# Kernel tuning notes

Measured on AMD Instinct MI355X. Metric: run time of the kernel, lower is better.

Reference implementation:

```python
import jax, jax.numpy as jnp
import numpy as np

N_NODES = 100000
N_EDGES = 3200000
IN_FEATS = 512
HIDDEN = 256
N_CLASSES = 64
NITER = 10
HALT_BIAS_INIT = 3.0


def setup_inputs() -> dict:
    key = jax.random.key(0)
    ks = jax.random.split(key, 8)
    x = jax.random.normal(ks[0], (N_NODES, IN_FEATS), dtype=jnp.float32)
    edge_index = jax.random.randint(ks[1], (2, N_EDGES), 0, N_NODES, dtype=jnp.int64)
    # Linear layers: layers[0]: in->hidden, layers[1]: hidden->classes, halt: classes->1
    W0 = jax.random.normal(ks[2], (IN_FEATS, HIDDEN), dtype=jnp.float32) / np.sqrt(IN_FEATS)
    b0 = jnp.zeros((HIDDEN,), dtype=jnp.float32)
    W1 = jax.random.normal(ks[3], (HIDDEN, N_CLASSES), dtype=jnp.float32) / np.sqrt(HIDDEN)
    b1 = jnp.zeros((N_CLASSES,), dtype=jnp.float32)
    Wh = jax.random.normal(ks[4], (N_CLASSES, 1), dtype=jnp.float32) / np.sqrt(N_CLASSES)
    bh = jnp.full((1,), HALT_BIAS_INIT, dtype=jnp.float32)
    return {"x": x, "edge_index": edge_index, "edge_dropout": 0,
            "W0": W0, "b0": b0, "W1": W1, "b1": b1, "Wh": Wh, "bh": bh}


def reference(x, edge_index, edge_dropout, W0, b0, W1, b1, Wh, bh):
    N = x.shape[0]
    # MLP encoder (eval mode: dropout is identity)
    h = jax.nn.relu(x @ W0 + b0)
    h = h @ W1 + b1                                   # [N, C]

    # gcn_norm with self-loops (edge_dropout=0 in eval => identical every iter)
    loops = jnp.arange(N, dtype=edge_index.dtype)
    row = jnp.concatenate([edge_index[0], loops])     # source
    col = jnp.concatenate([edge_index[1], loops])     # target (aggregation index)
    deg = jax.ops.segment_sum(jnp.ones_like(col, dtype=h.dtype), col, num_segments=N)
    dinv = jnp.where(deg > 0, deg ** -0.5, 0.0)
    norm = dinv[row] * dinv[col]                      # [E+N]

    def step(ph, _):
        msg = norm[:, None] * ph[row]                 # gather + scale, [E+N, C]
        ph2 = jax.ops.segment_sum(msg, col, num_segments=N)  # scatter_add
        logit = jnp.clip(ph2 @ Wh + bh, -10.0, 10.0)  # [N, 1]
        return ph2, (ph2, logit)

    _, (props, logits) = jax.lax.scan(step, h, None, length=NITER)
    outputs = jnp.concatenate([h[None], props], axis=0)       # [niter+1, N, C]
    halting_logits = jnp.transpose(logits[:, :, 0])           # [N, niter]

    lam = jax.nn.sigmoid(halting_logits)
    remain = jnp.cumprod(1.0 - lam, axis=1)                   # inclusive
    remain_excl = jnp.concatenate([jnp.ones((N, 1), lam.dtype), remain[:, :-1]], axis=1)
    p = lam * remain_excl
    p = p.at[:, -1].add(remain[:, -1])                        # leftover mass to last step
    return outputs, p, halting_logits
```

## Files before the change

### kernel.cpp

```cpp
#include <hip/hip_runtime.h>
#include <hip/hip_bf16.h>

#define N_NODES  100000
#define N_EDGES  3200000
#define IN_FEATS 512
#define HIDDEN   256
#define N_CLASSES 64
#define NITER    10

#define SCAN_NB  49

#define OUT_P_OFF  ((size_t)(NITER + 1) * N_NODES * N_CLASSES)
#define OUT_HL_OFF (OUT_P_OFF + (size_t)N_NODES * NITER)

#define WS_META_INTS (4 * N_NODES + 128)
#define WS_CSR_OFF   ((size_t)WS_META_INTS * 4)
#define WS_W0F_OFF   (WS_CSR_OFF + (size_t)2 * N_EDGES * 4)
#define WS_W1F_OFF   (WS_W0F_OFF + 262144)
#define WS_SH0_OFF   (WS_W1F_OFF + 32768)
#define WS_SH1_OFF   (WS_SH0_OFF + (size_t)N_NODES * 64 * 2)
#define WS_NEED_W    (WS_SH0_OFF)
#define WS_NEED_BF   (WS_SH1_OFF + (size_t)N_NODES * 64 * 2)

typedef _Float16 f16x8 __attribute__((ext_vector_type(8)));
typedef _Float16 f16x4 __attribute__((ext_vector_type(4)));
typedef float    f32x4 __attribute__((ext_vector_type(4)));

__device__ __forceinline__ float bflo(unsigned v) { return __uint_as_float(v << 16); }
__device__ __forceinline__ float bfhi(unsigned v) { return __uint_as_float(v & 0xffff0000u); }
__device__ __forceinline__ unsigned short f2bf(float f) {
    unsigned u = __float_as_uint(f);
    return (unsigned short)((u + 0x7fffu + ((u >> 16) & 1u)) >> 16);
}

__global__ void k_detect(const int* ei, int* flag) {
    if (threadIdx.x == 0 && blockIdx.x == 0) {
        int is64 = 1;
        for (int k = 0; k < 128; ++k) {
            if (ei[2 * k + 1] != 0) { is64 = 0; break; }
        }
        *flag = is64;
    }
}

__device__ __forceinline__ int edge_row(const void* ei, int is64, int e) {
    return is64 ? (int)((const long long*)ei)[e] : ((const int*)ei)[e];
}
__device__ __forceinline__ int edge_col(const void* ei, int is64, int e) {
    return is64 ? (int)((const long long*)ei)[(size_t)N_EDGES + e]
                : ((const int*)ei)[(size_t)N_EDGES + e];
}

__global__ void k_count(const void* ei, const int* flag, int* cnt) {
    int e = blockIdx.x * 256 + threadIdx.x;
    if (e >= N_EDGES) return;
    int is64 = *flag;
    atomicAdd(&cnt[edge_col(ei, is64, e)], 1);
}

__global__ __launch_bounds__(256) void k_scan1(const int* cnt, int* part) {
    __shared__ int sd[256];
    int b = blockIdx.x, t = threadIdx.x;
    int s = 0;
    for (int j = t; j < 2048; j += 256) {
        int idx = b * 2048 + j;
        if (idx < N_NODES) s += cnt[idx];
    }
    sd[t] = s;
    __syncthreads();
    for (int o = 128; o > 0; o >>= 1) {
        if (t < o) sd[t] += sd[t + o];
        __syncthreads();
    }
    if (t == 0) part[b] = sd[0];
}

__global__ __launch_bounds__(256) void k_scan2(int* part, int* offs) {
    __shared__ int sd[256];
    int t = threadIdx.x;
    sd[t] = (t < SCAN_NB) ? part[t] : 0;
    __syncthreads();
    for (int o = 1; o < 256; o <<= 1) {
        int add = (t >= o) ? sd[t - o] : 0;
        __syncthreads();
        sd[t] += add;
        __syncthreads();
    }
    if (t < SCAN_NB) part[t] = (t == 0) ? 0 : sd[t - 1];
    if (t == 0) offs[N_NODES] = N_EDGES;
}

__global__ __launch_bounds__(256) void k_scan3(const int* cnt, const int* part, int* offs) {
    __shared__ int sd[256];
    int b = blockIdx.x, t = threadIdx.x;
    int base = b * 2048 + t * 8;
    int local[8];
    int s = 0;
#pragma unroll
    for (int j = 0; j < 8; ++j) {
        int idx = base + j;
        int v = (idx < N_NODES) ? cnt[idx] : 0;
        local[j] = s;
        s += v;
    }
    sd[t] = s;
    __syncthreads();
    for (int o = 1; o < 256; o <<= 1) {
        int add = (t >= o) ? sd[t - o] : 0;
        __syncthreads();
        sd[t] += add;
        __syncthreads();
    }
    int tbase = part[b] + ((t == 0) ? 0 : sd[t - 1]);
#pragma unroll
    for (int j = 0; j < 8; ++j) {
        int idx = base + j;
        if (idx < N_NODES) offs[idx] = tbase + local[j];
    }
}

__global__ void k_dinv(const int* cnt, float* dinv) {
    int i = blockIdx.x * 256 + threadIdx.x;
    if (i >= N_NODES) return;
    dinv[i] = rsqrtf((float)(cnt[i] + 1));
}

__global__ void k_fill(const void* ei, const int* flag, const float* dinv,
                       const int* offs, int* cursor, int2* csr) {
    int e = blockIdx.x * 256 + threadIdx.x;
    if (e >= N_EDGES) return;
    int is64 = *flag;
    int r = edge_row(ei, is64, e);
    int c = edge_col(ei, is64, e);
    int pos = offs[c] + atomicAdd(&cursor[c], 1);
    csr[pos] = make_int2(r, __float_as_int(dinv[r] * dinv[c]));
}

__global__ void k_prep_w(const float* __restrict__ W0, const float* __restrict__ W1,
                         _Float16* __restrict__ W0f, _Float16* __restrict__ W1f) {
    int id = blockIdx.x * 256 + threadIdx.x;
    if (id < 16384) {
        int l = id & 63, c = (id >> 6) & 15, kkg = id >> 10;
        int n = c * 16 + (l & 15);
        int kb = kkg * 32 + ((l >> 4) * 8);
        f16x8 v;
#pragma unroll
        for (int j = 0; j < 8; ++j) v[j] = (_Float16)W0[(size_t)(kb + j) * HIDDEN + n];
        *(f16x8*)&W0f[(size_t)id * 8] = v;
    } else if (id < 16384 + 2048) {
        int id2 = id - 16384;
        int l = id2 & 63, c = (id2 >> 6) & 3, kkg = id2 >> 8;
        int n = c * 16 + (l & 15);
        int kb = kkg * 32 + ((l >> 4) * 8);
        f16x8 v;
#pragma unroll
        for (int j = 0; j < 8; ++j) v[j] = (_Float16)W1[(size_t)(kb + j) * N_CLASSES + n];
        *(f16x8*)&W1f[(size_t)id2 * 8] = v;
    }
}

#define EBM 64
#define XS_STRIDE 72
#define H1_STRIDE 264
#define XS0   0
#define XS1   9216
#define WST0  18432
#define WST1  34816
#define W2ST0 34816
#define W2ST1 38912
__global__ __launch_bounds__(256) void k_encoder_mfma(
        const float* __restrict__ x, const _Float16* __restrict__ W0f,
        const float* __restrict__ b0, const _Float16* __restrict__ W1f,
        const float* __restrict__ b1, float* __restrict__ out,
        unsigned short* __restrict__ shadow, int write_shadow) {
    __shared__ char smem[51200];
    const int t = threadIdx.x;
    const int w = t >> 6, l = t & 63;
    const int g = l >> 4, r15 = l & 15;
    const int row0 = blockIdx.x * EBM;
    const int c4 = t & 15;
    const int srow0 = t >> 4;

    f32x4 acc[16];
#pragma unroll
    for (int c = 0; c < 16; ++c) acc[c] = (f32x4){0.f, 0.f, 0.f, 0.f};

    float4 xld[4];
    f16x8 wld[4];
#pragma unroll
    for (int q = 0; q < 4; ++q) {
        int grow = row0 + q * 16 + srow0;
        if (grow >= N_NODES) grow = N_NODES - 1;
        xld[q] = *(const float4*)&x[(size_t)grow * IN_FEATS + c4 * 4];
    }
#pragma unroll
    for (int q = 0; q < 4; ++q) wld[q] = *(const f16x8*)&W0f[(size_t)(q * 256 + t) * 8];
#pragma unroll
    for (int q = 0; q < 4; ++q) {
        f16x4 hv = {(_Float16)xld[q].x, (_Float16)xld[q].y, (_Float16)xld[q].z, (_Float16)xld[q].w};
        *(f16x4*)(smem + XS0 + ((q * 16 + srow0) * XS_STRIDE + c4 * 4) * 2) = hv;
    }
#pragma unroll
    for (int q = 0; q < 4; ++q)
        *(f16x8*)(smem + WST0 + (q * 256 + t) * 16) = wld[q];
    __syncthreads();

    for (int kkg = 0; kkg < 16; ++kkg) {
        const int kc = kkg >> 1, kk = kkg & 1;
        if (kkg < 15) {
#pragma unroll
            for (int q = 0; q < 4; ++q)
                wld[q] = *(const f16x8*)&W0f[(size_t)((kkg + 1) * 1024 + q * 256 + t) * 8];
        }
        if (kk == 0 && kc < 7) {
#pragma unroll
            for (int q = 0; q < 4; ++q) {
                int grow = row0 + q * 16 + srow0;
                if (grow >= N_NODES) grow = N_NODES - 1;
                xld[q] = *(const float4*)&x[(size_t)grow * IN_FEATS + (kc + 1) * 64 + c4 * 4];
            }
        }
        const char* xbase = smem + ((kc & 1) ? XS1 : XS0);
        const char* wbase = smem + ((kkg & 1) ? WST1 : WST0);
        f16x8 af = *(const f16x8*)(xbase + ((w * 16 + r15) * XS_STRIDE + kk * 32 + g * 8) * 2);
#pragma unroll
        for (int c = 0; c < 16; ++c) {
            f16x8 bf = *(const f16x8*)(wbase + ((c << 6) | l) * 16);
            acc[c] = __builtin_amdgcn_mfma_f32_16x16x32_f16(af, bf, acc[c], 0, 0, 0);
        }
        if (kkg < 15) {
            char* wdst = smem + ((kkg & 1) ? WST0 : WST1);
#pragma unroll
            for (int q = 0; q < 4; ++q)
                *(f16x8*)(wdst + (q * 256 + t) * 16) = wld[q];
        }
        if (kk == 1 && kc < 7) {
            char* xdst = smem + ((kc & 1) ? XS0 : XS1);
#pragma unroll
            for (int q = 0; q < 4; ++q) {
                f16x4 hv = {(_Float16)xld[q].x, (_Float16)xld[q].y, (_Float16)xld[q].z, (_Float16)xld[q].w};
                *(f16x4*)(xdst + ((q * 16 + srow0) * XS_STRIDE + c4 * 4) * 2) = hv;
            }
        }
        __syncthreads();
    }

    f16x8 w2ld = *(const f16x8*)&W1f[(size_t)t * 8];
#pragma unroll
    for (int c = 0; c < 16; ++c) {
        float bb = b0[c * 16 + r15];
#pragma unroll
        for (int i = 0; i < 4; ++i) {
            int row = w * 16 + g * 4 + i;
            *(_Float16*)(smem + (row * H1_STRIDE + c * 16 + r15) * 2) =
                (_Float16)fmaxf(acc[c][i] + bb, 0.f);
        }
    }
    *(f16x8*)(smem + W2ST0 + t * 16) = w2ld;
    __syncthreads();

    f32x4 acc2[4];
#pragma unroll
    for (int c = 0; c < 4; ++c) acc2[c] = (f32x4){0.f, 0.f, 0.f, 0.f};
    for (int kkg = 0; kkg < 8; ++kkg) {
        if (kkg < 7) w2ld = *(const f16x8*)&W1f[(size_t)((kkg + 1) * 256 + t) * 8];
        const char* wbase = smem + ((kkg & 1) ? W2ST1 : W2ST0);
        f16x8 af = *(const f16x8*)(smem + ((w * 16 + r15) * H1_STRIDE + kkg * 32 + g * 8) * 2);
#pragma unroll
        for (int c = 0; c < 4; ++c) {
            f16x8 bf = *(const f16x8*)(wbase + ((c << 6) | l) * 16);
            acc2[c] = __builtin_amdgcn_mfma_f32_16x16x32_f16(af, bf, acc2[c], 0, 0, 0);
        }
        if (kkg < 7)
            *(f16x8*)(smem + ((kkg & 1) ? W2ST0 : W2ST1) + t * 16) = w2ld;
        __syncthreads();
    }
#pragma unroll
    for (int c = 0; c < 4; ++c) {
        float bb = b1[c * 16 + r15];
#pragma unroll
        for (int i = 0; i < 4; ++i) {
            int row = row0 + w * 16 + g * 4 + i;
            if (row < N_NODES) {
                float v = acc2[c][i] + bb;
                int col = c * 16 + r15;
                out[(size_t)row * 64 + col] = v;
                if (write_shadow) shadow[(size_t)row * 64 + col] = f2bf(v);
            }
        }
    }
}

__global__ __launch_bounds__(256) void k_encoder(const float* __restrict__ x,
        const float* __restrict__ W0, const float* __restrict__ b0,
        const float* __restrict__ W1, const float* __restrict__ b1,
        float* __restrict__ out) {
    __shared__ float xsh[32][128];
    __shared__ float h1s[32][HIDDEN + 1];
    const int t = threadIdx.x;
    const int rg = t >> 6;
    const int cg = t & 63;
    const size_t row0 = (size_t)blockIdx.x * 32;
    float acc[8][4];
#pragma unroll
    for (int i = 0; i < 8; ++i)
        acc[i][0] = acc[i][1] = acc[i][2] = acc[i][3] = 0.f;
    for (int kc = 0; kc < 4; ++kc) {
        __syncthreads();
#pragma unroll
        for (int q = 0; q < 4; ++q) {
            int idx = t + q * 256;
            int r = idx >> 5, pos = idx & 31;
            *(float4*)&xsh[r][pos * 4] =
                *(const float4*)&x[(row0 + r) * IN_FEATS + kc * 128 + pos * 4];
        }
        __syncthreads();
        for (int kk = 0; kk < 128; kk += 4) {
            float4 xv[8];
#pragma unroll
            for (int i = 0; i < 8; ++i) xv[i] = *(const float4*)&xsh[rg * 8 + i][kk];
#pragma unroll
            for (int j = 0; j < 4; ++j) {
                float4 wv = *(const float4*)&W0[(size_t)(kc * 128 + kk + j) * HIDDEN + cg * 4];
#pragma unroll
                for (int i = 0; i < 8; ++i) {
                    float xj = (&xv[i].x)[j];
                    acc[i][0] = fmaf(xj, wv.x, acc[i][0]);
                    acc[i][1] = fmaf(xj, wv.y, acc[i][1]);
                    acc[i][2] = fmaf(xj, wv.z, acc[i][2]);
                    acc[i][3] = fmaf(xj, wv.w, acc[i][3]);
                }
            }
        }
    }
    float4 bb = *(const float4*)&b0[cg * 4];
#pragma unroll
    for (int i = 0; i < 8; ++i) {
        int r = rg * 8 + i;
        h1s[r][cg * 4 + 0] = fmaxf(acc[i][0] + bb.x, 0.f);
        h1s[r][cg * 4 + 1] = fmaxf(acc[i][1] + bb.y, 0.f);
        h1s[r][cg * 4 + 2] = fmaxf(acc[i][2] + bb.z, 0.f);
        h1s[r][cg * 4 + 3] = fmaxf(acc[i][3] + bb.w, 0.f);
    }
    __syncthreads();
    float a2[8];
#pragma unroll
    for (int i = 0; i < 8; ++i) a2[i] = 0.f;
    for (int k = 0; k < HIDDEN; ++k) {
        float wv = W1[(size_t)k * N_CLASSES + cg];
#pragma unroll
        for (int i = 0; i < 8; ++i) a2[i] = fmaf(h1s[rg * 8 + i][k], wv, a2[i]);
    }
    float bv = b1[cg];
#pragma unroll
    for (int i = 0; i < 8; ++i)
        out[(row0 + rg * 8 + i) * N_CLASSES + cg] = a2[i] + bv;
}

__global__ __launch_bounds__(256) void k_prop_bf(
        const unsigned short* __restrict__ pin_bf, float* __restrict__ pout,
        unsigned short* __restrict__ pout_bf, const int* __restrict__ offs,
        const int2* __restrict__ csr, const float* __restrict__ dinv,
        const float* __restrict__ Wh, const float* __restrict__ bh,
        float* __restrict__ hl, int t) {
    int node = (blockIdx.x * 256 + threadIdx.x) >> 5;
    if (node >= N_NODES) return;
    int hlane = threadIdx.x & 31;
    int base = threadIdx.x & 32;
    float di = dinv[node];
    unsigned vs = *(const unsigned*)&pin_bf[(size_t)node * 64 + hlane * 2];
    float a0 = di * di * bflo(vs), a1 = di * di * bfhi(vs);
    float c0 = 0.f, c1 = 0.f;
    int e0 = offs[node], e1 = offs[node + 1];
    for (int eb = e0; eb < e1; eb += 32) {
        int n = e1 - eb; if (n > 32) n = 32;
        int idx = eb + hlane;
        int2 ew = csr[idx < e1 ? idx : e1 - 1];
        int j = 0;
        for (; j + 8 <= n; j += 8) {
            unsigned v[8]; float w[8];
#pragma unroll
            for (int q = 0; q < 8; ++q) {
                int s = __shfl(ew.x, base + j + q, 64);
                w[q] = __int_as_float(__shfl(ew.y, base + j + q, 64));
                v[q] = *(const unsigned*)&pin_bf[(size_t)s * 64 + hlane * 2];
            }
#pragma unroll
            for (int q = 0; q < 8; ++q) {
                if (q & 1) { c0 = fmaf(w[q], bflo(v[q]), c0); c1 = fmaf(w[q], bfhi(v[q]), c1); }
                else       { a0 = fmaf(w[q], bflo(v[q]), a0); a1 = fmaf(w[q], bfhi(v[q]), a1); }
            }
        }
        for (; j < n; ++j) {
            int s = __shfl(ew.x, base + j, 64);
            float w = __int_as_float(__shfl(ew.y, base + j, 64));
            unsigned v = *(const unsigned*)&pin_bf[(size_t)s * 64 + hlane * 2];
            a0 = fmaf(w, bflo(v), a0);
            a1 = fmaf(w, bfhi(v), a1);
        }
    }
    float fa = a0 + c0, fb = a1 + c1;
    *(float2*)&pout[(size_t)node * 64 + hlane * 2] = make_float2(fa, fb);
    *(unsigned*)&pout_bf[(size_t)node * 64 + hlane * 2] =
        (unsigned)f2bf(fa) | ((unsigned)f2bf(fb) << 16);
    float2 wh = *(const float2*)&Wh[hlane * 2];
    float s = fa * wh.x + fb * wh.y;
#pragma unroll
    for (int o = 16; o > 0; o >>= 1) s += __shfl_xor(s, o, 64);
    if (hlane == 0) {
        float lg = s + bh[0];
        lg = fminf(10.0f, fmaxf(-10.0f, lg));
        hl[(size_t)node * NITER + t] = lg;
    }
}

__global__ __launch_bounds__(256) void k_prop(const float* __restrict__ pin,
        float* __restrict__ pout, const int* __restrict__ offs,
        const int2* __restrict__ csr, const float* __restrict__ dinv,
        const float* __restrict__ Wh, const float* __restrict__ bh,
        float* __restrict__ hl, int t) {
    int wid = (blockIdx.x * blockDim.x + threadIdx.x) >> 6;
    int lane = threadIdx.x & 63;
    if (wid >= N_NODES) return;
    float di = dinv[wid];
    float a[4];
    a[0] = di * di * pin[(size_t)wid * 64 + lane];
    a[1] = a[2] = a[3] = 0.f;
    int e0 = offs[wid], e1 = offs[wid + 1];
    for (int eb = e0; eb < e1; eb += 64) {
        int n = e1 - eb; if (n > 64) n = 64;
        int idx = eb + lane;
        int2 ew = csr[idx < e1 ? idx : e1 - 1];
        int j = 0;
        for (; j + 8 <= n; j += 8) {
            float v[8], w[8];
#pragma unroll
            for (int q = 0; q < 8; ++q) {
                int s = __shfl(ew.x, j + q, 64);
                w[q] = __int_as_float(__shfl(ew.y, j + q, 64));
                v[q] = pin[(size_t)s * 64 + lane];
            }
#pragma unroll
            for (int q = 0; q < 8; ++q) a[q & 3] = fmaf(w[q], v[q], a[q & 3]);
        }
        for (; j < n; ++j) {
            int s = __shfl(ew.x, j, 64);
            float w = __int_as_float(__shfl(ew.y, j, 64));
            a[0] = fmaf(w, pin[(size_t)s * 64 + lane], a[0]);
        }
    }
    float acc = (a[0] + a[1]) + (a[2] + a[3]);
    pout[(size_t)wid * 64 + lane] = acc;
    float s = acc * Wh[lane];
#pragma unroll
    for (int o = 32; o > 0; o >>= 1) s += __shfl_xor(s, o, 64);
    if (lane == 0) {
        float lg = s + bh[0];
        lg = fminf(10.0f, fmaxf(-10.0f, lg));
        hl[(size_t)wid * NITER + t] = lg;
    }
}

__global__ void k_p(const float* __restrict__ hl, float* __restrict__ p) {
    int i = blockIdx.x * 256 + threadIdx.x;
    if (i >= N_NODES) return;
    float remain = 1.0f;
    float pv[NITER];
#pragma unroll
    for (int t = 0; t < NITER; ++t) {
        float lg = hl[(size_t)i * NITER + t];
        float lam = 1.0f / (1.0f + expf(-lg));
        pv[t] = lam * remain;
        remain *= (1.0f - lam);
    }
    pv[NITER - 1] += remain;
#pragma unroll
    for (int t = 0; t < NITER; ++t) p[(size_t)i * NITER + t] = pv[t];
}

extern "C" void kernel_launch(void* const* d_in, const int* in_sizes, int n_in,
                              void* d_out, int out_size, void* d_ws, size_t ws_size,
                              hipStream_t stream) {
    const float* x  = (const float*)d_in[0];
    const void*  ei = d_in[1];
    const float* W0 = (const float*)d_in[3];
    const float* b0 = (const float*)d_in[4];
    const float* W1 = (const float*)d_in[5];
    const float* b1 = (const float*)d_in[6];
    const float* Wh = (const float*)d_in[7];
    const float* bh = (const float*)d_in[8];
    float* out = (float*)d_out;

    int* ws_i   = (int*)d_ws;
    int* cnt    = ws_i;
    int* offs   = ws_i + N_NODES;
    int* cursor = ws_i + 2 * N_NODES + 2;
    int* part   = ws_i + 3 * N_NODES + 2;
    int* flag   = ws_i + 3 * N_NODES + 66;
    float* dinv = (float*)(ws_i + 3 * N_NODES + 128);
    int2* csr   = (int2*)((char*)d_ws + WS_CSR_OFF);
    _Float16* W0f = (_Float16*)((char*)d_ws + WS_W0F_OFF);
    _Float16* W1f = (_Float16*)((char*)d_ws + WS_W1F_OFF);
    unsigned short* sh0 = (unsigned short*)((char*)d_ws + WS_SH0_OFF);
    unsigned short* sh1 = (unsigned short*)((char*)d_ws + WS_SH1_OFF);

    const int use_w  = ws_size >= WS_NEED_W;
    const int use_bf = ws_size >= WS_NEED_BF;

    hipMemsetAsync(d_ws, 0, (size_t)(3 * N_NODES + 128) * 4, stream);
    k_detect<<<1, 64, 0, stream>>>((const int*)ei, flag);
    k_count<<<(N_EDGES + 255) / 256, 256, 0, stream>>>(ei, flag, cnt);
    k_scan1<<<SCAN_NB, 256, 0, stream>>>(cnt, part);
    k_scan2<<<1, 256, 0, stream>>>(part, offs);
    k_scan3<<<SCAN_NB, 256, 0, stream>>>(cnt, part, offs);
    k_dinv<<<(N_NODES + 255) / 256, 256, 0, stream>>>(cnt, dinv);
    k_fill<<<(N_EDGES + 255) / 256, 256, 0, stream>>>(ei, flag, dinv, offs, cursor, csr);

    if (use_w) {
        k_prep_w<<<72, 256, 0, stream>>>(W0, W1, W0f, W1f);
        k_encoder_mfma<<<(N_NODES + EBM - 1) / EBM, 256, 0, stream>>>(
            x, W0f, b0, W1f, b1, out, sh0, use_bf);
    } else {
        k_encoder<<<N_NODES / 32, 256, 0, stream>>>(x, W0, b0, W1, b1, out);
    }

    float* hl = out + OUT_HL_OFF;
    if (use_bf) {
        for (int it = 0; it < NITER; ++it) {
            const unsigned short* pin_bf = (it & 1) ? sh1 : sh0;
            unsigned short* pout_bf      = (it & 1) ? sh0 : sh1;
            float* pout = out + (size_t)(it + 1) * N_NODES * N_CLASSES;
            k_prop_bf<<<((size_t)N_NODES * 32 + 255) / 256, 256, 0, stream>>>(
                pin_bf, pout, pout_bf, offs, csr, dinv, Wh, bh, hl, it);
        }
    } else {
        for (int it = 0; it < NITER; ++it) {
            const float* pin = out + (size_t)it * N_NODES * N_CLASSES;
            float* pout      = out + (size_t)(it + 1) * N_NODES * N_CLASSES;
            k_prop<<<((size_t)N_NODES * 64 + 255) / 256, 256, 0, stream>>>(
                pin, pout, offs, csr, dinv, Wh, bh, hl, it);
        }
    }
    k_p<<<(N_NODES + 255) / 256, 256, 0, stream>>>(hl, out + OUT_P_OFF);
}
```

Before: 1.020 ms.

## Partition CSR fill by destination range and unroll propagation gather by 16

The CSR fill kernel now runs a grid-stride loop where each block group (blockIdx & 7) handles only edges whose target falls in one eighth of the node range. With round-robin block-to-XCD dispatch, this keeps atomics and CSR writes for a node range local to one XCD's L2. Every group re-reads the column indices, so edge-index reads go up by about eight times. Separately, the propagation gather loop gains a 16-wide unrolled stage to put more independent loads in flight per wavefront, at the cost of higher register pressure.

```diff
diff --git a/kernel.cpp b/kernel.cpp
--- a/kernel.cpp
+++ b/kernel.cpp
@@ -125,15 +125,23 @@
     dinv[i] = rsqrtf((float)(cnt[i] + 1));
 }
 
-__global__ void k_fill(const void* ei, const int* flag, const float* dinv,
-                       const int* offs, int* cursor, int2* csr) {
-    int e = blockIdx.x * 256 + threadIdx.x;
-    if (e >= N_EDGES) return;
-    int is64 = *flag;
-    int r = edge_row(ei, is64, e);
-    int c = edge_col(ei, is64, e);
-    int pos = offs[c] + atomicAdd(&cursor[c], 1);
-    csr[pos] = make_int2(r, __float_as_int(dinv[r] * dinv[c]));
+#define FILL_GRID 3200
+__global__ __launch_bounds__(256) void k_fill_part(const void* ei, const int* flag,
+        const float* dinv, const int* offs, int* cursor, int2* csr) {
+    const int g = blockIdx.x & 7;
+    const int bi = blockIdx.x >> 3;
+    const int lo = g * (N_NODES / 8);
+    const int hi = lo + (N_NODES / 8);
+    const int is64 = *flag;
+    const int stride = (FILL_GRID >> 3) * 256;
+    for (int e = bi * 256 + threadIdx.x; e < N_EDGES; e += stride) {
+        int c = edge_col(ei, is64, e);
+        if (c >= lo && c < hi) {
+            int r = edge_row(ei, is64, e);
+            int pos = offs[c] + atomicAdd(&cursor[c], 1);
+            csr[pos] = make_int2(r, __float_as_int(dinv[r] * dinv[c]));
+        }
+    }
 }
 
 __global__ void k_prep_w(const float* __restrict__ W0, const float* __restrict__ W1,
@@ -377,6 +385,20 @@
         int idx = eb + hlane;
         int2 ew = csr[idx < e1 ? idx : e1 - 1];
         int j = 0;
+        for (; j + 16 <= n; j += 16) {
+            unsigned v[16]; float w[16];
+#pragma unroll
+            for (int q = 0; q < 16; ++q) {
+                int s = __shfl(ew.x, base + j + q, 64);
+                w[q] = __int_as_float(__shfl(ew.y, base + j + q, 64));
+                v[q] = *(const unsigned*)&pin_bf[(size_t)s * 64 + hlane * 2];
+            }
+#pragma unroll
+            for (int q = 0; q < 16; ++q) {
+                if (q & 1) { c0 = fmaf(w[q], bflo(v[q]), c0); c1 = fmaf(w[q], bfhi(v[q]), c1); }
+                else       { a0 = fmaf(w[q], bflo(v[q]), a0); a1 = fmaf(w[q], bfhi(v[q]), a1); }
+            }
+        }
         for (; j + 8 <= n; j += 8) {
             unsigned v[8]; float w[8];
 #pragma unroll
@@ -514,7 +536,7 @@
     k_scan2<<<1, 256, 0, stream>>>(part, offs);
     k_scan3<<<SCAN_NB, 256, 0, stream>>>(cnt, part, offs);
     k_dinv<<<(N_NODES + 255) / 256, 256, 0, stream>>>(cnt, dinv);
-    k_fill<<<(N_EDGES + 255) / 256, 256, 0, stream>>>(ei, flag, dinv, offs, cursor, csr);
+    k_fill_part<<<FILL_GRID, 256, 0, stream>>>(ei, flag, dinv, offs, cursor, csr);
 
     if (use_w) {
         k_prep_w<<<72, 256, 0, stream>>>(W0, W1, W0f, W1f);
```

Result: slower. 1.065 ms (+4.3%).

## Prescale bf16 shadow by dinv and store byte-offset-only CSR

Applied to the files above, without the earlier changes.

The GCN normalization is factored so the bf16 shadow holds dinv[src]*h. Aggregation then becomes a plain sum, scaled once by dinv[dst] at the end. The CSR now stores only the source index pre-shifted to a byte offset (int instead of int2), which halves edge-list traffic and removes the per-edge weight shuffle and FMA; a 16-wide unrolled gather is also added. The cost is an extra rounding of the prescaled values, the fallback path must now re-gather dinv per edge, and the shifted index limits node count to fit in 32 bits after the shift.

```diff
diff --git a/kernel.cpp b/kernel.cpp
--- a/kernel.cpp
+++ b/kernel.cpp
@@ -125,15 +125,15 @@
     dinv[i] = rsqrtf((float)(cnt[i] + 1));
 }
 
-__global__ void k_fill(const void* ei, const int* flag, const float* dinv,
-                       const int* offs, int* cursor, int2* csr) {
+__global__ void k_fill(const void* ei, const int* flag,
+                       const int* offs, int* cursor, int* csr) {
     int e = blockIdx.x * 256 + threadIdx.x;
     if (e >= N_EDGES) return;
     int is64 = *flag;
     int r = edge_row(ei, is64, e);
     int c = edge_col(ei, is64, e);
     int pos = offs[c] + atomicAdd(&cursor[c], 1);
-    csr[pos] = make_int2(r, __float_as_int(dinv[r] * dinv[c]));
+    csr[pos] = r << 7;
 }
 
 __global__ void k_prep_w(const float* __restrict__ W0, const float* __restrict__ W1,
@@ -172,6 +172,7 @@
         const float* __restrict__ x, const _Float16* __restrict__ W0f,
         const float* __restrict__ b0, const _Float16* __restrict__ W1f,
         const float* __restrict__ b1, float* __restrict__ out,
+        const float* __restrict__ dinv,
         unsigned short* __restrict__ shadow, int write_shadow) {
     __shared__ char smem[51200];
     const int t = threadIdx.x;
@@ -285,7 +286,8 @@
                 float v = acc2[c][i] + bb;
                 int col = c * 16 + r15;
                 out[(size_t)row * 64 + col] = v;
-                if (write_shadow) shadow[(size_t)row * 64 + col] = f2bf(v);
+                if (write_shadow)
+                    shadow[(size_t)row * 64 + col] = f2bf(dinv[row] * v);
             }
         }
     }
@@ -357,52 +359,64 @@
         out[(row0 + rg * 8 + i) * N_CLASSES + cg] = a2[i] + bv;
 }
 
-__global__ __launch_bounds__(256) void k_prop_bf(
-        const unsigned short* __restrict__ pin_bf, float* __restrict__ pout,
-        unsigned short* __restrict__ pout_bf, const int* __restrict__ offs,
-        const int2* __restrict__ csr, const float* __restrict__ dinv,
+__global__ __launch_bounds__(256) void k_prop_s(
+        const unsigned short* __restrict__ pin_s, float* __restrict__ pout,
+        unsigned short* __restrict__ pout_s, const int* __restrict__ offs,
+        const int* __restrict__ csr, const float* __restrict__ dinv,
         const float* __restrict__ Wh, const float* __restrict__ bh,
         float* __restrict__ hl, int t) {
     int node = (blockIdx.x * 256 + threadIdx.x) >> 5;
     if (node >= N_NODES) return;
     int hlane = threadIdx.x & 31;
     int base = threadIdx.x & 32;
-    float di = dinv[node];
-    unsigned vs = *(const unsigned*)&pin_bf[(size_t)node * 64 + hlane * 2];
-    float a0 = di * di * bflo(vs), a1 = di * di * bfhi(vs);
+    const char* gbase = (const char*)pin_s + hlane * 4;
+    unsigned own = *(const unsigned*)(gbase + ((size_t)node << 7));
+    float a0 = bflo(own), a1 = bfhi(own);
     float c0 = 0.f, c1 = 0.f;
     int e0 = offs[node], e1 = offs[node + 1];
     for (int eb = e0; eb < e1; eb += 32) {
         int n = e1 - eb; if (n > 32) n = 32;
         int idx = eb + hlane;
-        int2 ew = csr[idx < e1 ? idx : e1 - 1];
+        int ew = csr[idx < e1 ? idx : e1 - 1];
         int j = 0;
+        for (; j + 16 <= n; j += 16) {
+            unsigned v[16];
+#pragma unroll
+            for (int q = 0; q < 16; ++q) {
+                int s = __shfl(ew, base + j + q, 64);
+                v[q] = *(const unsigned*)(gbase + s);
+            }
+#pragma unroll
+            for (int q = 0; q < 16; ++q) {
+                if (q & 1) { c0 += bflo(v[q]); c1 += bfhi(v[q]); }
+                else       { a0 += bflo(v[q]); a1 += bfhi(v[q]); }
+            }
+        }
         for (; j + 8 <= n; j += 8) {
-            unsigned v[8]; float w[8];
+            unsigned v[8];
 #pragma unroll
             for (int q = 0; q < 8; ++q) {
-                int s = __shfl(ew.x, base + j + q, 64);
-                w[q] = __int_as_float(__shfl(ew.y, base + j + q, 64));
-                v[q] = *(const unsigned*)&pin_bf[(size_t)s * 64 + hlane * 2];
+                int s = __shfl(ew, base + j + q, 64);
+                v[q] = *(const unsigned*)(gbase + s);
             }
 #pragma unroll
             for (int q = 0; q < 8; ++q) {
-                if (q & 1) { c0 = fmaf(w[q], bflo(v[q]), c0); c1 = fmaf(w[q], bfhi(v[q]), c1); }
-                else       { a0 = fmaf(w[q], bflo(v[q]), a0); a1 = fmaf(w[q], bfhi(v[q]), a1); }
+                if (q & 1) { c0 += bflo(v[q]); c1 += bfhi(v[q]); }
+                else       { a0 += bflo(v[q]); a1 += bfhi(v[q]); }
             }
         }
         for (; j < n; ++j) {
-            int s = __shfl(ew.x, base + j, 64);
-            float w = __int_as_float(__shfl(ew.y, base + j, 64));
-            unsigned v = *(const unsigned*)&pin_bf[(size_t)s * 64 + hlane * 2];
-            a0 = fmaf(w, bflo(v), a0);
-            a1 = fmaf(w, bfhi(v), a1);
-        }
-    }
-    float fa = a0 + c0, fb = a1 + c1;
+            int s = __shfl(ew, base + j, 64);
+            unsigned v = *(const unsigned*)(gbase + s);
+            a0 += bflo(v);
+            a1 += bfhi(v);
+        }
+    }
+    float di = dinv[node];
+    float fa = di * (a0 + c0), fb = di * (a1 + c1);
     *(float2*)&pout[(size_t)node * 64 + hlane * 2] = make_float2(fa, fb);
-    *(unsigned*)&pout_bf[(size_t)node * 64 + hlane * 2] =
-        (unsigned)f2bf(fa) | ((unsigned)f2bf(fb) << 16);
+    *(unsigned*)&pout_s[(size_t)node * 64 + hlane * 2] =
+        (unsigned)f2bf(di * fa) | ((unsigned)f2bf(di * fb) << 16);
     float2 wh = *(const float2*)&Wh[hlane * 2];
     float s = fa * wh.x + fb * wh.y;
 #pragma unroll
@@ -416,7 +430,7 @@
 
 __global__ __launch_bounds__(256) void k_prop(const float* __restrict__ pin,
         float* __restrict__ pout, const int* __restrict__ offs,
-        const int2* __restrict__ csr, const float* __restrict__ dinv,
+        const int* __restrict__ csr, const float* __restrict__ dinv,
         const float* __restrict__ Wh, const float* __restrict__ bh,
         float* __restrict__ hl, int t) {
     int wid = (blockIdx.x * blockDim.x + threadIdx.x) >> 6;
@@ -430,23 +444,22 @@
     for (int eb = e0; eb < e1; eb += 64) {
         int n = e1 - eb; if (n > 64) n = 64;
         int idx = eb + lane;
-        int2 ew = csr[idx < e1 ? idx : e1 - 1];
+        int ew = csr[idx < e1 ? idx : e1 - 1];
         int j = 0;
         for (; j + 8 <= n; j += 8) {
             float v[8], w[8];
 #pragma unroll
             for (int q = 0; q < 8; ++q) {
-                int s = __shfl(ew.x, j + q, 64);
-                w[q] = __int_as_float(__shfl(ew.y, j + q, 64));
-                v[q] = pin[(size_t)s * 64 + lane];
+                int r = __shfl(ew, j + q, 64) >> 7;
+                w[q] = dinv[r] * di;
+                v[q] = pin[(size_t)r * 64 + lane];
             }
 #pragma unroll
             for (int q = 0; q < 8; ++q) a[q & 3] = fmaf(w[q], v[q], a[q & 3]);
         }
         for (; j < n; ++j) {
-            int s = __shfl(ew.x, j, 64);
-            float w = __int_as_float(__shfl(ew.y, j, 64));
-            a[0] = fmaf(w, pin[(size_t)s * 64 + lane], a[0]);
+            int r = __shfl(ew, j, 64) >> 7;
+            a[0] = fmaf(dinv[r] * di, pin[(size_t)r * 64 + lane], a[0]);
         }
     }
     float acc = (a[0] + a[1]) + (a[2] + a[3]);
@@ -498,7 +511,7 @@
     int* part   = ws_i + 3 * N_NODES + 2;
     int* flag   = ws_i + 3 * N_NODES + 66;
     float* dinv = (float*)(ws_i + 3 * N_NODES + 128);
-    int2* csr   = (int2*)((char*)d_ws + WS_CSR_OFF);
+    int* csr    = (int*)((char*)d_ws + WS_CSR_OFF);
     _Float16* W0f = (_Float16*)((char*)d_ws + WS_W0F_OFF);
     _Float16* W1f = (_Float16*)((char*)d_ws + WS_W1F_OFF);
     unsigned short* sh0 = (unsigned short*)((char*)d_ws + WS_SH0_OFF);
@@ -514,12 +527,12 @@
     k_scan2<<<1, 256, 0, stream>>>(part, offs);
     k_scan3<<<SCAN_NB, 256, 0, stream>>>(cnt, part, offs);
     k_dinv<<<(N_NODES + 255) / 256, 256, 0, stream>>>(cnt, dinv);
-    k_fill<<<(N_EDGES + 255) / 256, 256, 0, stream>>>(ei, flag, dinv, offs, cursor, csr);
+    k_fill<<<(N_EDGES + 255) / 256, 256, 0, stream>>>(ei, flag, offs, cursor, csr);
 
     if (use_w) {
         k_prep_w<<<72, 256, 0, stream>>>(W0, W1, W0f, W1f);
         k_encoder_mfma<<<(N_NODES + EBM - 1) / EBM, 256, 0, stream>>>(
-            x, W0f, b0, W1f, b1, out, sh0, use_bf);
+            x, W0f, b0, W1f, b1, out, dinv, sh0, use_bf);
     } else {
         k_encoder<<<N_NODES / 32, 256, 0, stream>>>(x, W0, b0, W1, b1, out);
     }
@@ -527,11 +540,11 @@
     float* hl = out + OUT_HL_OFF;
     if (use_bf) {
         for (int it = 0; it < NITER; ++it) {
-            const unsigned short* pin_bf = (it & 1) ? sh1 : sh0;
-            unsigned short* pout_bf      = (it & 1) ? sh0 : sh1;
+            const unsigned short* pin_s = (it & 1) ? sh1 : sh0;
+            unsigned short* pout_s      = (it & 1) ? sh0 : sh1;
             float* pout = out + (size_t)(it + 1) * N_NODES * N_CLASSES;
-            k_prop_bf<<<((size_t)N_NODES * 32 + 255) / 256, 256, 0, stream>>>(
-                pin_bf, pout, pout_bf, offs, csr, dinv, Wh, bh, hl, it);
+            k_prop_s<<<((size_t)N_NODES * 32 + 255) / 256, 256, 0, stream>>>(
+                pin_s, pout, pout_s, offs, csr, dinv, Wh, bh, hl, it);
         }
     } else {
         for (int it = 0; it < NITER; ++it) {
```

Result: faster. 992.2 us (-2.8%).
